# Performance work log

Measured on AMD Instinct MI355X. Metric: run time of the kernel, lower is better.

Reference implementation:

```python
import jax, jax.numpy as jnp
import numpy as np

NUM_HEADS = 4
GROUPS = 8
EPS = 1e-5


def group_norm(x, w, b):
    B, C, H, W = x.shape
    xg = x.reshape(B, GROUPS, C // GROUPS, H, W)
    mu = jnp.mean(xg, axis=(2, 3, 4), keepdims=True)
    var = jnp.var(xg, axis=(2, 3, 4), keepdims=True)
    xg = (xg - mu) * jax.lax.rsqrt(var + EPS)
    x = xg.reshape(B, C, H, W)
    return x * w[None, :, None, None] + b[None, :, None, None]


def setup_inputs() -> dict:
    key = jax.random.key(0)
    k1, k2, k3 = jax.random.split(key, 3)
    B, C, H, W = 16, 256, 32, 32
    x = jax.random.normal(k1, (B, C, H, W), dtype=jnp.float32)
    gn_w = jnp.ones((C,), dtype=jnp.float32)
    gn_b = jnp.zeros((C,), dtype=jnp.float32)
    qkv_w = jax.random.normal(k2, (3 * C, C), dtype=jnp.float32) * 0.02
    qkv_b = jnp.zeros((3 * C,), dtype=jnp.float32)
    proj_w = jax.random.normal(k3, (C, C), dtype=jnp.float32) * 0.02
    proj_b = jnp.zeros((C,), dtype=jnp.float32)
    return {"x": x, "gn_w": gn_w, "gn_b": gn_b, "qkv_w": qkv_w,
            "qkv_b": qkv_b, "proj_w": proj_w, "proj_b": proj_b}


def reference(x, gn_w, gn_b, qkv_w, qkv_b, proj_w, proj_b):
    B, C, H, W = x.shape
    Dh = C // NUM_HEADS
    N = H * W
    skip = x
    xn = group_norm(x, gn_w, gn_b)
    # 1x1 conv QKV projection: [B,3C,H,W]
    qkv = jnp.einsum('oc,bchw->bohw', qkv_w, xn) + qkv_b[None, :, None, None]
    # split channel dim 3C -> [3, heads, Dh], flatten spatial -> N
    qkv = qkv.reshape(B, 3, NUM_HEADS, Dh, N)
    qkv = jnp.transpose(qkv, (1, 0, 2, 4, 3))  # [3,B,heads,N,Dh]
    q, k, v = qkv[0], qkv[1], qkv[2]
    scale = 1.0 / np.sqrt(Dh).astype(np.float32)
    attn = jnp.einsum('bhnd,bhmd->bhnm', q, k) * scale  # [B,heads,N,N]
    attn = jax.nn.softmax(attn, axis=-1)
    out = jnp.einsum('bhnm,bhmd->bhnd', attn, v)  # [B,heads,N,Dh]
    out = jnp.transpose(out, (0, 1, 3, 2)).reshape(B, C, H, W)
    out = jnp.einsum('oc,bchw->bohw', proj_w, out) + proj_b[None, :, None, None]
    return out + skip
```

## Files before the change

kernel.cpp:

```cpp
#include <hip/hip_runtime.h>

typedef unsigned short u16;
typedef __bf16 bf16x8 __attribute__((ext_vector_type(8)));
typedef float f32x4 __attribute__((ext_vector_type(4)));
typedef float f32x16 __attribute__((ext_vector_type(16)));

#define QSCALE 0.18033688011112042f

__device__ __forceinline__ u16 f2bf(float f) {
  __bf16 h = (__bf16)f;
  union { __bf16 b; u16 u; } cv;
  cv.b = h;
  return cv.u;
}
__device__ __forceinline__ unsigned pack2(float a, float b) {
#if __has_builtin(__builtin_amdgcn_cvt_pk_bf16_f32)
  typedef __bf16 bf16x2 __attribute__((ext_vector_type(2)));
  bf16x2 p = __builtin_amdgcn_cvt_pk_bf16_f32(a, b);
  union { bf16x2 v; unsigned u; } cv;
  cv.v = p;
  return cv.u;
#else
  return (unsigned)f2bf(a) | ((unsigned)f2bf(b) << 16);
#endif
}
__device__ __forceinline__ float fexp2(float x) {
  return __builtin_amdgcn_exp2f(x);
}
__device__ __forceinline__ void cp16(const u16* g, u16* l) {
  __builtin_amdgcn_global_load_lds(
      (const __attribute__((address_space(1))) void*)g,
      (__attribute__((address_space(3))) void*)l, 16, 0, 0);
}

__global__ __launch_bounds__(256) void prep(
    const float* __restrict__ qw, const float* __restrict__ pw,
    const float* __restrict__ x,
    u16* __restrict__ qwb, u16* __restrict__ pwb, float* __restrict__ stats) {
  __shared__ float sh1[256], sh2[256];
  const int blk = blockIdx.x;
  const int t = threadIdx.x;
  if (blk < 256) {
    int i = blk * 256 + t;
    const float* s; u16* d; int j;
    if (i < 49152) { s = qw; d = qwb; j = i; }
    else           { s = pw; d = pwb; j = i - 49152; }
    float4 v = *(const float4*)(s + (size_t)j * 4);
    uint2 o; o.x = pack2(v.x, v.y); o.y = pack2(v.z, v.w);
    *(uint2*)(d + (size_t)j * 4) = o;
    return;
  }
  const int bid = blk - 256;
  int cl = t >> 3;
  int off = (t & 7) * 4;
  const float* p = x + (size_t)bid * 32768 + (size_t)cl * 1024 + off;
  float s = 0.f, ss = 0.f;
#pragma unroll 8
  for (int i = 0; i < 32; ++i) {
    float4 v = *(const float4*)(p + i * 32);
    s += v.x + v.y + v.z + v.w;
    ss += v.x * v.x + v.y * v.y + v.z * v.z + v.w * v.w;
  }
  sh1[t] = s; sh2[t] = ss;
  __syncthreads();
  for (int st = 128; st > 0; st >>= 1) {
    if (t < st) { sh1[t] += sh1[t + st]; sh2[t] += sh2[t + st]; }
    __syncthreads();
  }
  if (t == 0) {
    float mean = sh1[0] * (1.f / 32768.f);
    float var = sh2[0] * (1.f / 32768.f) - mean * mean;
    stats[bid * 2] = mean;
    stats[bid * 2 + 1] = rsqrtf(var + 1e-5f);
  }
}

__global__ __launch_bounds__(256) void gemm_qkv(
    const u16* __restrict__ A, const float* __restrict__ x,
    const float* __restrict__ stats,
    const float* __restrict__ gw, const float* __restrict__ gb,
    const float* __restrict__ bias,
    u16* __restrict__ o_q, u16* __restrict__ o_k, u16* __restrict__ o_v) {
  const int l = blockIdx.x;
  const int xcd = l & 7;
  const int i2 = l >> 3;
  const int m_t = i2 % 6;
  const int nl6 = i2 / 6;
  const int nt = xcd * 16 + nl6;
  const int m0 = m_t * 128;
  const int n0 = nt * 128;
  const int b = nt >> 3;
  const int nsp0 = (nt & 7) * 128;

  const int t = threadIdx.x;
  const int wave = t >> 6, lane = t & 63, lm = lane & 15, quad = lane >> 4;
  const int wr = wave >> 1, wc = wave & 1;

  __shared__ u16 As[2][128 * 32];
  __shared__ u16 Bs[2][128 * 32];

  f32x4 acc[4][4];
  const f32x4 fzero = {0.f, 0.f, 0.f, 0.f};
#pragma unroll
  for (int i = 0; i < 4; ++i)
#pragma unroll
    for (int j = 0; j < 4; ++j) acc[i][j] = fzero;

  const int srow = t >> 2, scol = (t & 3) * 8;
  const u16* pA0 = A + (size_t)(m0 + srow) * 256 + scol;
  const u16* pA1 = A + (size_t)(m0 + 64 + srow) * 256 + scol;

  const int n2 = t & 63, gq = t >> 6;
  const float* xb = x + (size_t)b * 262144 + nsp0 + 2 * n2;
  const int gsw = (gq ^ (n2 & 3)) * 8;

  float2 vB[8];
  uint4 vA0, vA1;

#define LD_B(ki)                                                       \
  {                                                                    \
    const int cb = (ki) * 32 + gq * 8;                                 \
    _Pragma("unroll") for (int i = 0; i < 8; ++i)                      \
        vB[i] = *(const float2*)(xb + (size_t)(cb + i) * 1024);        \
  }
#define ST_B(ki, buf)                                                  \
  {                                                                    \
    const int cb = (ki) * 32 + gq * 8;                                 \
    const float mu = stats[(b * 8 + (ki)) * 2];                        \
    const float rq = stats[(b * 8 + (ki)) * 2 + 1];                    \
    float e0[8], e1[8];                                                \
    _Pragma("unroll") for (int i = 0; i < 8; ++i) {                    \
      const float w = gw[cb + i] * rq;                                 \
      const float bb = gb[cb + i] - mu * w;                            \
      e0[i] = vB[i].x * w + bb;                                        \
      e1[i] = vB[i].y * w + bb;                                        \
    }                                                                  \
    uint4 w0, w1;                                                      \
    w0.x = pack2(e0[0], e0[1]); w0.y = pack2(e0[2], e0[3]);            \
    w0.z = pack2(e0[4], e0[5]); w0.w = pack2(e0[6], e0[7]);            \
    w1.x = pack2(e1[0], e1[1]); w1.y = pack2(e1[2], e1[3]);            \
    w1.z = pack2(e1[4], e1[5]); w1.w = pack2(e1[6], e1[7]);            \
    *(uint4*)(Bs[buf] + (2 * n2) * 32 + gsw) = w0;                     \
    *(uint4*)(Bs[buf] + (2 * n2 + 1) * 32 + gsw) = w1;                 \
  }

  LD_B(0);
  vA0 = *(const uint4*)pA0;
  vA1 = *(const uint4*)pA1;
  ST_B(0, 0);
  *(uint4*)(As[0] + srow * 32 + scol) = vA0;
  *(uint4*)(As[0] + (64 + srow) * 32 + scol) = vA1;
  LD_B(1);
  vA0 = *(const uint4*)(pA0 + 32);
  vA1 = *(const uint4*)(pA1 + 32);

  for (int ki = 0; ki < 8; ++ki) {
    __syncthreads();
    if (ki + 1 < 8) {
      ST_B(ki + 1, (ki + 1) & 1);
      u16* as = As[(ki + 1) & 1];
      *(uint4*)(as + srow * 32 + scol) = vA0;
      *(uint4*)(as + (64 + srow) * 32 + scol) = vA1;
    }
    if (ki + 2 < 8) {
      LD_B(ki + 2);
      vA0 = *(const uint4*)(pA0 + (ki + 2) * 32);
      vA1 = *(const uint4*)(pA1 + (ki + 2) * 32);
    }
    const u16* as = As[ki & 1];
    const u16* bs = Bs[ki & 1];
    bf16x8 af[4], bf[4];
#pragma unroll
    for (int mb = 0; mb < 4; ++mb)
      af[mb] = *(const bf16x8*)(as + (wr * 64 + mb * 16 + lm) * 32 + quad * 8);
#pragma unroll
    for (int nb = 0; nb < 4; ++nb) {
      const int row = wc * 64 + nb * 16 + lm;
      bf[nb] = *(const bf16x8*)(bs + row * 32 + ((quad ^ ((row >> 1) & 3)) * 8));
    }
#pragma unroll
    for (int mb = 0; mb < 4; ++mb)
#pragma unroll
      for (int nb = 0; nb < 4; ++nb)
        acc[mb][nb] = __builtin_amdgcn_mfma_f32_16x16x32_bf16(af[mb], bf[nb],
                                                              acc[mb][nb], 0, 0, 0);
  }
#undef LD_B
#undef ST_B

#pragma unroll
  for (int mb = 0; mb < 4; ++mb) {
#pragma unroll
    for (int nb = 0; nb < 4; ++nb) {
      const int o = m0 + wr * 64 + mb * 16 + 4 * quad;
      const int ng = n0 + wc * 64 + nb * 16 + lm;
      const int bb = ng >> 10, n = ng & 1023;
      const int kind = o >> 8;
      const int h = (o >> 6) & 3;
      const int dd = o & 63;
      const int jc = n >> 6, jl = n & 63;
      const size_t bhoff = ((size_t)(bb * 4 + h)) * 65536 + jc * 4096;
      if (kind <= 1) {
        const float sc = (kind == 0) ? QSCALE : 1.f;
        u16* base = (kind == 0) ? o_q : o_k;
        ushort4 pq;
        pq.x = f2bf((acc[mb][nb][0] + bias[o]) * sc);
        pq.y = f2bf((acc[mb][nb][1] + bias[o + 1]) * sc);
        pq.z = f2bf((acc[mb][nb][2] + bias[o + 2]) * sc);
        pq.w = f2bf((acc[mb][nb][3] + bias[o + 3]) * sc);
        *(ushort4*)(base + bhoff + jl * 64 + (((dd >> 3) ^ (jl & 7)) * 8) +
                    (dd & 7)) = pq;
      } else {
        u16* vbase = o_v + bhoff + (jl & 7);
#pragma unroll
        for (int r = 0; r < 4; ++r) {
          const int d = dd + r;
          vbase[d * 64 + (((jl >> 3) ^ (d & 7)) * 8)] =
              f2bf(acc[mb][nb][r] + bias[o + r]);
        }
      }
    }
  }
}

__global__ __launch_bounds__(256) void gemm_proj(
    const u16* __restrict__ A, const u16* __restrict__ Bm,
    const float* __restrict__ bias,
    const float* __restrict__ skip, float* __restrict__ out) {
  const int m0 = blockIdx.y * 64;
  const int n0 = blockIdx.x * 128;
  const int t = threadIdx.x;
  const int wave = t >> 6, lane = t & 63, lm = lane & 15, quad = lane >> 4;
  const int wr = wave >> 1, wc = wave & 1;

  __shared__ u16 As[2][64 * 32];
  __shared__ u16 Bs[2][128 * 32];

  f32x4 acc[2][4];
  const f32x4 fzero = {0.f, 0.f, 0.f, 0.f};
#pragma unroll
  for (int i = 0; i < 2; ++i)
#pragma unroll
    for (int j = 0; j < 4; ++j) acc[i][j] = fzero;

  const int srow = t >> 2, scol = (t & 3) * 8;
  const u16* pA0 = A + (size_t)(m0 + srow) * 256 + scol;
  const u16* pB0 = Bm + (size_t)(n0 + srow) * 256 + scol;
  const u16* pB1 = Bm + (size_t)(n0 + 64 + srow) * 256 + scol;

  uint4 pa0 = *(const uint4*)pA0;
  uint4 pb0 = *(const uint4*)pB0;
  uint4 pb1 = *(const uint4*)pB1;
  *(uint4*)(As[0] + srow * 32 + scol) = pa0;
  *(uint4*)(Bs[0] + srow * 32 + scol) = pb0;
  *(uint4*)(Bs[0] + (64 + srow) * 32 + scol) = pb1;
  pa0 = *(const uint4*)(pA0 + 32);
  pb0 = *(const uint4*)(pB0 + 32);
  pb1 = *(const uint4*)(pB1 + 32);

  for (int ki = 0; ki < 8; ++ki) {
    __syncthreads();
    if (ki + 1 < 8) {
      u16* as = As[(ki + 1) & 1];
      u16* bs = Bs[(ki + 1) & 1];
      *(uint4*)(as + srow * 32 + scol) = pa0;
      *(uint4*)(bs + srow * 32 + scol) = pb0;
      *(uint4*)(bs + (64 + srow) * 32 + scol) = pb1;
    }
    if (ki + 2 < 8) {
      const int ko = (ki + 2) * 32;
      pa0 = *(const uint4*)(pA0 + ko);
      pb0 = *(const uint4*)(pB0 + ko);
      pb1 = *(const uint4*)(pB1 + ko);
    }
    const u16* as = As[ki & 1];
    const u16* bs = Bs[ki & 1];
    bf16x8 af[2], bf[4];
#pragma unroll
    for (int mb = 0; mb < 2; ++mb)
      af[mb] = *(const bf16x8*)(as + (wr * 32 + mb * 16 + lm) * 32 + quad * 8);
#pragma unroll
    for (int nb = 0; nb < 4; ++nb)
      bf[nb] = *(const bf16x8*)(bs + (wc * 64 + nb * 16 + lm) * 32 + quad * 8);
#pragma unroll
    for (int mb = 0; mb < 2; ++mb)
#pragma unroll
      for (int nb = 0; nb < 4; ++nb)
        acc[mb][nb] = __builtin_amdgcn_mfma_f32_16x16x32_bf16(af[mb], bf[nb],
                                                              acc[mb][nb], 0, 0, 0);
  }

#pragma unroll
  for (int mb = 0; mb < 2; ++mb) {
#pragma unroll
    for (int nb = 0; nb < 4; ++nb) {
      const int o = m0 + wr * 32 + mb * 16 + 4 * quad;
      const int ng = n0 + wc * 64 + nb * 16 + lm;
      const int b = ng >> 10, n = ng & 1023;
#pragma unroll
      for (int r = 0; r < 4; ++r) {
        const size_t oi = ((size_t)(b * 256 + o + r)) * 1024 + n;
        out[oi] = acc[mb][nb][r] + bias[o + r] + skip[oi];
      }
    }
  }
}

__global__ __launch_bounds__(256) void attn_fused(
    const u16* __restrict__ qsw, const u16* __restrict__ ksw,
    const u16* __restrict__ vsw, u16* __restrict__ att) {
  const int bid = blockIdx.x;
  const int bh = (bid & 7) * 8 + ((bid >> 3) & 7);
  const int qtile = bid >> 6;
  const int t = threadIdx.x;
  const int wave = t >> 6, lane = t & 63;
  const int l5 = lane & 31, h = lane >> 5;
  const int iblk = wave & 1, jh = wave >> 1;

  const u16* qb = qsw + (size_t)bh * 65536 + qtile * 4096;
  const u16* kb = ksw + (size_t)bh * 65536;
  const u16* vb = vsw + (size_t)bh * 65536;

  __shared__ u16 KV[2][2][4096];
  __shared__ u16 QP[4096];

  const int t8 = t * 8;
  cp16(qb + t8, QP + t8);
  cp16(qb + 2048 + t8, QP + 2048 + t8);
  cp16(kb + t8, KV[0][0] + t8);
  cp16(kb + 2048 + t8, KV[0][0] + 2048 + t8);
  cp16(vb + t8, KV[0][1] + t8);
  cp16(vb + 2048 + t8, KV[0][1] + 2048 + t8);
  __syncthreads();

  const int qrow = iblk * 32 + l5;
  bf16x8 qf[4];
#pragma unroll
  for (int sd = 0; sd < 4; ++sd)
    qf[sd] = *(const bf16x8*)(QP + qrow * 64 + (((2 * sd + h) ^ (qrow & 7)) * 8));
  __syncthreads();

  u16* Pw = QP + wave * 1024;
  const int pswz = (l5 >> 1) & 3;

  f32x16 oacc0, oacc1;
#pragma unroll
  for (int r = 0; r < 16; ++r) { oacc0[r] = 0.f; oacc1[r] = 0.f; }
  float lp = 0.f;

  for (int jc = 0; jc < 16; ++jc) {
    if (jc) __syncthreads();
    if (jc + 1 < 16) {
      const int base = (jc + 1) * 4096;
      u16* kd = KV[(jc + 1) & 1][0];
      u16* vd = KV[(jc + 1) & 1][1];
      cp16(kb + base + t8, kd + t8);
      cp16(kb + base + 2048 + t8, kd + 2048 + t8);
      cp16(vb + base + t8, vd + t8);
      cp16(vb + base + 2048 + t8, vd + 2048 + t8);
    }
    const u16* Ks = KV[jc & 1][0];
    const u16* Vs = KV[jc & 1][1];

    f32x16 sacc;
#pragma unroll
    for (int r = 0; r < 16; ++r) sacc[r] = 0.f;
    const int krow = jh * 32 + l5;
    const int kswz = krow & 7;
#pragma unroll
    for (int sd = 0; sd < 4; ++sd) {
      bf16x8 kf = *(const bf16x8*)(Ks + krow * 64 + (((2 * sd + h) ^ kswz) * 8));
      sacc = __builtin_amdgcn_mfma_f32_32x32x16_bf16(kf, qf[sd], sacc, 0, 0, 0);
    }
#pragma unroll
    for (int g = 0; g < 4; ++g) {
      const float e0 = fexp2(sacc[4 * g + 0]);
      const float e1 = fexp2(sacc[4 * g + 1]);
      const float e2 = fexp2(sacc[4 * g + 2]);
      const float e3 = fexp2(sacc[4 * g + 3]);
      lp += (e0 + e1) + (e2 + e3);
      uint2 pw;
      pw.x = pack2(e0, e1);
      pw.y = pack2(e2, e3);
      *(uint2*)(Pw + l5 * 32 + ((g ^ pswz) * 8) + 4 * h) = pw;
    }
    bf16x8 pf[2];
#pragma unroll
    for (int sj = 0; sj < 2; ++sj)
      pf[sj] = *(const bf16x8*)(Pw + l5 * 32 + (((2 * sj + h) ^ pswz) * 8));
#pragma unroll
    for (int sj = 0; sj < 2; ++sj) {
      const int vrow0 = l5;
      const int vrow1 = 32 + l5;
      const int gv = 4 * jh + 2 * sj + h;
      bf16x8 vf0 = *(const bf16x8*)(Vs + vrow0 * 64 + ((gv ^ (vrow0 & 7)) * 8));
      bf16x8 vf1 = *(const bf16x8*)(Vs + vrow1 * 64 + ((gv ^ (vrow1 & 7)) * 8));
      oacc0 = __builtin_amdgcn_mfma_f32_32x32x16_bf16(vf0, pf[sj], oacc0, 0, 0, 0);
      oacc1 = __builtin_amdgcn_mfma_f32_32x32x16_bf16(vf1, pf[sj], oacc1, 0, 0, 0);
    }
  }

  lp += __shfl_xor(lp, 32);

  float* cb = (float*)KV[0];
  __syncthreads();
  if (jh == 1) {
    float* d = cb + (iblk * 64 + lane) * 33;
#pragma unroll
    for (int r = 0; r < 16; ++r) { d[r] = oacc0[r]; d[16 + r] = oacc1[r]; }
    d[32] = lp;
  }
  __syncthreads();
  if (jh == 0) {
    const float* s = cb + (iblk * 64 + lane) * 33;
#pragma unroll
    for (int r = 0; r < 16; ++r) { oacc0[r] += s[r]; oacc1[r] += s[16 + r]; }
    lp += s[32];
    const float inv = 1.f / lp;
    const int b = bh >> 2, hh = bh & 3;
    const int n = qtile * 64 + iblk * 32 + l5;
    u16* obase = att + ((size_t)(b * 1024 + n)) * 256 + hh * 64;
#pragma unroll
    for (int g = 0; g < 4; ++g) {
      ushort4 o0, o1;
      o0.x = f2bf(oacc0[4 * g + 0] * inv);
      o0.y = f2bf(oacc0[4 * g + 1] * inv);
      o0.z = f2bf(oacc0[4 * g + 2] * inv);
      o0.w = f2bf(oacc0[4 * g + 3] * inv);
      o1.x = f2bf(oacc1[4 * g + 0] * inv);
      o1.y = f2bf(oacc1[4 * g + 1] * inv);
      o1.z = f2bf(oacc1[4 * g + 2] * inv);
      o1.w = f2bf(oacc1[4 * g + 3] * inv);
      *(ushort4*)(obase + 8 * g + 4 * h) = o0;
      *(ushort4*)(obase + 32 + 8 * g + 4 * h) = o1;
    }
  }
}

extern "C" void kernel_launch(void* const* d_in, const int* in_sizes, int n_in,
                              void* d_out, int out_size, void* d_ws, size_t ws_size,
                              hipStream_t stream) {
  const float* x      = (const float*)d_in[0];
  const float* gn_w   = (const float*)d_in[1];
  const float* gn_b   = (const float*)d_in[2];
  const float* qkv_w  = (const float*)d_in[3];
  const float* qkv_b  = (const float*)d_in[4];
  const float* proj_w = (const float*)d_in[5];
  const float* proj_b = (const float*)d_in[6];
  float* out = (float*)d_out;

  char* ws = (char*)d_ws;
  float* stats = (float*)(ws + 0);
  u16* qwb = (u16*)(ws + 4096);
  u16* pwb = (u16*)(ws + 397312);
  u16* qsw = (u16*)(ws + 8916992);
  u16* ksw = (u16*)(ws + 17305600);
  u16* vsw = (u16*)(ws + 25694208);
  u16* att = (u16*)(ws + 34082816);

  prep<<<384, 256, 0, stream>>>(qkv_w, proj_w, x, qwb, pwb, stats);
  gemm_qkv<<<768, 256, 0, stream>>>(qwb, x, stats, gn_w, gn_b, qkv_b,
                                    qsw, ksw, vsw);
  attn_fused<<<1024, 256, 0, stream>>>(qsw, ksw, vsw, att);
  gemm_proj<<<dim3(128, 4), 256, 0, stream>>>(pwb, att, proj_b, x, out);
}
```

Baseline: 139.0 us.

## Precompute normalized transposed bf16 activations in prep kernel for QKV GEMM

The prep kernel now applies the group norm itself and writes a transposed bf16 [B,N,C] copy of the activations through an LDS tile, rather than only storing per-group statistics. The QKV GEMM then loads contiguous bf16 rows for its B operand. This drops the strided fp32 loads and per-tile normalize/convert work that each of the six M-tiles repeated on the same x data. In exchange the prep blocks do an extra full pass over x and write an 8 MB intermediate, with several syncthreads per tile.

```diff
diff --git a/kernel.cpp b/kernel.cpp
--- a/kernel.cpp
+++ b/kernel.cpp
@@ -33,11 +33,11 @@
       (__attribute__((address_space(3))) void*)l, 16, 0, 0);
 }
 
-__global__ __launch_bounds__(256) void prep(
+__global__ __launch_bounds__(256) void prep2(
     const float* __restrict__ qw, const float* __restrict__ pw,
     const float* __restrict__ x,
-    u16* __restrict__ qwb, u16* __restrict__ pwb, float* __restrict__ stats) {
-  __shared__ float sh1[256], sh2[256];
+    const float* __restrict__ gw, const float* __restrict__ gb,
+    u16* __restrict__ qwb, u16* __restrict__ pwb, u16* __restrict__ xnt) {
   const int blk = blockIdx.x;
   const int t = threadIdx.x;
   if (blk < 256) {
@@ -50,10 +50,16 @@
     *(uint2*)(d + (size_t)j * 4) = o;
     return;
   }
+  __shared__ float sh1[256], sh2[256];
+  __shared__ float s_mu, s_rq;
+  __shared__ float tile[32][129];
+
   const int bid = blk - 256;
-  int cl = t >> 3;
-  int off = (t & 7) * 4;
-  const float* p = x + (size_t)bid * 32768 + (size_t)cl * 1024 + off;
+  const int b = bid >> 3, g = bid & 7;
+  const float* xs = x + (size_t)bid * 32768;
+  const int cl = t >> 3;
+  const int off = (t & 7) * 4;
+  const float* p = xs + (size_t)cl * 1024 + off;
   float s = 0.f, ss = 0.f;
 #pragma unroll 8
   for (int i = 0; i < 32; ++i) {
@@ -70,15 +76,53 @@
   if (t == 0) {
     float mean = sh1[0] * (1.f / 32768.f);
     float var = sh2[0] * (1.f / 32768.f) - mean * mean;
-    stats[bid * 2] = mean;
-    stats[bid * 2 + 1] = rsqrtf(var + 1e-5f);
+    s_mu = mean;
+    s_rq = rsqrtf(var + 1e-5f);
+  }
+  __syncthreads();
+
+  const int c = g * 32 + cl;
+  const float w = gw[c] * s_rq;
+  const float bb = gb[c] - s_mu * w;
+  const int no = (t & 7) * 16;
+  u16* xrow = xnt + ((size_t)b * 1024) * 256 + g * 32;
+
+  for (int nt0 = 0; nt0 < 8; ++nt0) {
+    const float* q = xs + (size_t)cl * 1024 + nt0 * 128 + no;
+    float4 v0 = *(const float4*)(q);
+    float4 v1 = *(const float4*)(q + 4);
+    float4 v2 = *(const float4*)(q + 8);
+    float4 v3 = *(const float4*)(q + 12);
+    if (nt0) __syncthreads();
+    float* tr = &tile[cl][no];
+    tr[0] = v0.x * w + bb;  tr[1] = v0.y * w + bb;
+    tr[2] = v0.z * w + bb;  tr[3] = v0.w * w + bb;
+    tr[4] = v1.x * w + bb;  tr[5] = v1.y * w + bb;
+    tr[6] = v1.z * w + bb;  tr[7] = v1.w * w + bb;
+    tr[8] = v2.x * w + bb;  tr[9] = v2.y * w + bb;
+    tr[10] = v2.z * w + bb; tr[11] = v2.w * w + bb;
+    tr[12] = v3.x * w + bb; tr[13] = v3.y * w + bb;
+    tr[14] = v3.z * w + bb; tr[15] = v3.w * w + bb;
+    __syncthreads();
+    const int n = t >> 1;
+    const int ch = (t & 1) * 16;
+    uint4 w0, w1;
+    w0.x = pack2(tile[ch + 0][n], tile[ch + 1][n]);
+    w0.y = pack2(tile[ch + 2][n], tile[ch + 3][n]);
+    w0.z = pack2(tile[ch + 4][n], tile[ch + 5][n]);
+    w0.w = pack2(tile[ch + 6][n], tile[ch + 7][n]);
+    w1.x = pack2(tile[ch + 8][n], tile[ch + 9][n]);
+    w1.y = pack2(tile[ch + 10][n], tile[ch + 11][n]);
+    w1.z = pack2(tile[ch + 12][n], tile[ch + 13][n]);
+    w1.w = pack2(tile[ch + 14][n], tile[ch + 15][n]);
+    u16* dst = xrow + ((size_t)(nt0 * 128 + n)) * 256 + ch;
+    *(uint4*)dst = w0;
+    *(uint4*)(dst + 8) = w1;
   }
 }
 
 __global__ __launch_bounds__(256) void gemm_qkv(
-    const u16* __restrict__ A, const float* __restrict__ x,
-    const float* __restrict__ stats,
-    const float* __restrict__ gw, const float* __restrict__ gb,
+    const u16* __restrict__ A, const u16* __restrict__ xnt,
     const float* __restrict__ bias,
     u16* __restrict__ o_q, u16* __restrict__ o_k, u16* __restrict__ o_v) {
   const int l = blockIdx.x;
@@ -111,43 +155,27 @@
   const u16* pA1 = A + (size_t)(m0 + 64 + srow) * 256 + scol;
 
   const int n2 = t & 63, gq = t >> 6;
-  const float* xb = x + (size_t)b * 262144 + nsp0 + 2 * n2;
+  const u16* xb = xnt + ((size_t)(b * 1024) + nsp0) * 256;
   const int gsw = (gq ^ (n2 & 3)) * 8;
 
-  float2 vB[8];
-  uint4 vA0, vA1;
-
-#define LD_B(ki)                                                       \
-  {                                                                    \
-    const int cb = (ki) * 32 + gq * 8;                                 \
-    _Pragma("unroll") for (int i = 0; i < 8; ++i)                      \
-        vB[i] = *(const float2*)(xb + (size_t)(cb + i) * 1024);        \
-  }
-#define ST_B(ki, buf)                                                  \
-  {                                                                    \
-    const int cb = (ki) * 32 + gq * 8;                                 \
-    const float mu = stats[(b * 8 + (ki)) * 2];                        \
-    const float rq = stats[(b * 8 + (ki)) * 2 + 1];                    \
-    float e0[8], e1[8];                                                \
-    _Pragma("unroll") for (int i = 0; i < 8; ++i) {                    \
-      const float w = gw[cb + i] * rq;                                 \
-      const float bb = gb[cb + i] - mu * w;                            \
-      e0[i] = vB[i].x * w + bb;                                        \
-      e1[i] = vB[i].y * w + bb;                                        \
-    }                                                                  \
-    uint4 w0, w1;                                                      \
-    w0.x = pack2(e0[0], e0[1]); w0.y = pack2(e0[2], e0[3]);            \
-    w0.z = pack2(e0[4], e0[5]); w0.w = pack2(e0[6], e0[7]);            \
-    w1.x = pack2(e1[0], e1[1]); w1.y = pack2(e1[2], e1[3]);            \
-    w1.z = pack2(e1[4], e1[5]); w1.w = pack2(e1[6], e1[7]);            \
-    *(uint4*)(Bs[buf] + (2 * n2) * 32 + gsw) = w0;                     \
-    *(uint4*)(Bs[buf] + (2 * n2 + 1) * 32 + gsw) = w1;                 \
+  uint4 vB0, vB1, vA0, vA1;
+
+#define LD_B(ki)                                                        \
+  {                                                                     \
+    const int cb = (ki) * 32 + gq * 8;                                  \
+    vB0 = *(const uint4*)(xb + (size_t)(2 * n2) * 256 + cb);            \
+    vB1 = *(const uint4*)(xb + (size_t)(2 * n2 + 1) * 256 + cb);        \
+  }
+#define ST_B(buf)                                                       \
+  {                                                                     \
+    *(uint4*)(Bs[buf] + (2 * n2) * 32 + gsw) = vB0;                     \
+    *(uint4*)(Bs[buf] + (2 * n2 + 1) * 32 + gsw) = vB1;                 \
   }
 
   LD_B(0);
   vA0 = *(const uint4*)pA0;
   vA1 = *(const uint4*)pA1;
-  ST_B(0, 0);
+  ST_B(0);
   *(uint4*)(As[0] + srow * 32 + scol) = vA0;
   *(uint4*)(As[0] + (64 + srow) * 32 + scol) = vA1;
   LD_B(1);
@@ -157,7 +185,7 @@
   for (int ki = 0; ki < 8; ++ki) {
     __syncthreads();
     if (ki + 1 < 8) {
-      ST_B(ki + 1, (ki + 1) & 1);
+      ST_B((ki + 1) & 1);
       u16* as = As[(ki + 1) & 1];
       *(uint4*)(as + srow * 32 + scol) = vA0;
       *(uint4*)(as + (64 + srow) * 32 + scol) = vA1;
@@ -450,17 +478,16 @@
   float* out = (float*)d_out;
 
   char* ws = (char*)d_ws;
-  float* stats = (float*)(ws + 0);
   u16* qwb = (u16*)(ws + 4096);
   u16* pwb = (u16*)(ws + 397312);
+  u16* xnt = (u16*)(ws + 528384);
   u16* qsw = (u16*)(ws + 8916992);
   u16* ksw = (u16*)(ws + 17305600);
   u16* vsw = (u16*)(ws + 25694208);
   u16* att = (u16*)(ws + 34082816);
 
-  prep<<<384, 256, 0, stream>>>(qkv_w, proj_w, x, qwb, pwb, stats);
-  gemm_qkv<<<768, 256, 0, stream>>>(qwb, x, stats, gn_w, gn_b, qkv_b,
-                                    qsw, ksw, vsw);
+  prep2<<<384, 256, 0, stream>>>(qkv_w, proj_w, x, gn_w, gn_b, qwb, pwb, xnt);
+  gemm_qkv<<<768, 256, 0, stream>>>(qwb, xnt, qkv_b, qsw, ksw, vsw);
   attn_fused<<<1024, 256, 0, stream>>>(qsw, ksw, vsw, att);
   gemm_proj<<<dim3(128, 4), 256, 0, stream>>>(pwb, att, proj_b, x, out);
 }
```

Result: slower. 145.3 us (+4.6%).
